# Optimization experiments

Hardware: AMD Instinct MI355X
Metric: run time of the kernel (lower is better)

The kernel has to match this reference:

```python
import jax, jax.numpy as jnp
import numpy as np

B = 2_000_000
ND = 3

def _skew(v):
    # v: [B,3] -> [B,3,3] skew-symmetric matrix
    z = jnp.zeros_like(v[..., 0])
    r0 = jnp.stack([z, -v[..., 2], v[..., 1]], axis=-1)
    r1 = jnp.stack([v[..., 2], z, -v[..., 0]], axis=-1)
    r2 = jnp.stack([-v[..., 1], v[..., 0], z], axis=-1)
    return jnp.stack([r0, r1, r2], axis=-2)

def _rotmat(v):
    # Closed-form expm of skew(v) (Rodrigues). Mathematically identical to tf.linalg.expm.
    th2 = jnp.sum(v * v, axis=-1)                      # [B]
    th = jnp.sqrt(th2)
    small = th < 1e-6
    th_s = jnp.where(small, 1.0, th)
    th2_s = jnp.where(small, 1.0, th2)
    a = jnp.where(small, 1.0, jnp.sin(th) / th_s)      # sin(t)/t
    b = jnp.where(small, 0.5, (1.0 - jnp.cos(th)) / th2_s)  # (1-cos t)/t^2
    K = _skew(v)                                       # [B,3,3]
    I = jnp.eye(ND, dtype=v.dtype)
    return I + a[:, None, None] * K + b[:, None, None] * jnp.matmul(K, K)

def setup_inputs() -> dict:
    key = jax.random.key(0)
    k1, k2, k3, k4 = jax.random.split(key, 4)
    trans = jax.random.normal(k1, (B, ND), dtype=jnp.float32)
    rotat = jax.random.normal(k2, (B, ND), dtype=jnp.float32)
    scal_dir = jax.random.normal(k3, (B, ND), dtype=jnp.float32)
    scal = jax.random.normal(k4, (B, ND), dtype=jnp.float32)
    return {"trans": trans, "rotat": rotat, "scal_dir": scal_dir, "scal": scal}

def reference(trans, rotat, scal_dir, scal):
    R = _rotmat(rotat)          # [B,3,3] rotation
    U = _rotmat(scal_dir)       # [B,3,3] scaling direction
    D = jnp.exp(scal)           # expm(diag(s)) == diag(exp(s)), [B,3]
    # U @ diag(D) @ U^T, then R @ (.)
    Ut = jnp.swapaxes(U, -1, -2)
    M = jnp.matmul(U, D[:, :, None] * Ut)   # diag(D) @ U^T broadcast as row-scaling
    M = jnp.matmul(R, M)
    return jnp.concatenate([M, trans[:, :, None]], axis=2)  # [B,3,4]
```

## Files before the change

### kernel.cpp

```cpp
#include <hip/hip_runtime.h>
#include <math.h>

#define TPB 256

__device__ __forceinline__ void rodrigues(float v0, float v1, float v2, float R[9]) {
    float th2 = v0 * v0 + v1 * v1 + v2 * v2;
    float th  = sqrtf(th2);
    float s, c;
    sincosf(th, &s, &c);
    bool  sm = th < 1e-6f;
    float a  = sm ? 1.0f : s / th;
    float b  = sm ? 0.5f : (1.0f - c) / th2;
    float cc = 1.0f - b * th2;
    R[0] = cc + b * v0 * v0;      R[1] = b * v0 * v1 - a * v2;  R[2] = b * v0 * v2 + a * v1;
    R[3] = b * v0 * v1 + a * v2;  R[4] = cc + b * v1 * v1;      R[5] = b * v1 * v2 - a * v0;
    R[6] = b * v0 * v2 - a * v1;  R[7] = b * v1 * v2 + a * v0;  R[8] = cc + b * v2 * v2;
}

__global__ __launch_bounds__(TPB) void aff_kernel(
    const float4* __restrict__ trans,
    const float4* __restrict__ rotat,
    const float4* __restrict__ sdir,
    const float4* __restrict__ scal,
    float4* __restrict__ out,
    int B)
{
    __shared__ float s_in[4][TPB * 3];
    __shared__ float s_out[TPB * 12];

    const int tid  = threadIdx.x;
    const int base = blockIdx.x * TPB;
    const int n    = min(TPB, B - base);
    const int nf4  = (n * 3) >> 2;

    if (tid < nf4) {
        const int gbase = (base * 3) >> 2;
        float4 a = trans[gbase + tid];
        float4 b = rotat[gbase + tid];
        float4 c = sdir [gbase + tid];
        float4 d = scal [gbase + tid];
        ((float4*)&s_in[0][0])[tid] = a;
        ((float4*)&s_in[1][0])[tid] = b;
        ((float4*)&s_in[2][0])[tid] = c;
        ((float4*)&s_in[3][0])[tid] = d;
    }
    __syncthreads();

    if (tid < n) {
        float t0 = s_in[0][3*tid+0], t1 = s_in[0][3*tid+1], t2 = s_in[0][3*tid+2];

        float R[9], U[9];
        rodrigues(s_in[1][3*tid+0], s_in[1][3*tid+1], s_in[1][3*tid+2], R);
        rodrigues(s_in[2][3*tid+0], s_in[2][3*tid+1], s_in[2][3*tid+2], U);
        float d0 = expf(s_in[3][3*tid+0]);
        float d1 = expf(s_in[3][3*tid+1]);
        float d2 = expf(s_in[3][3*tid+2]);

        float W[9];
#pragma unroll
        for (int i = 0; i < 3; ++i) {
            W[3*i+0] = U[3*i+0] * d0;
            W[3*i+1] = U[3*i+1] * d1;
            W[3*i+2] = U[3*i+2] * d2;
        }
        float S[9];
#pragma unroll
        for (int i = 0; i < 3; ++i)
#pragma unroll
            for (int j = 0; j < 3; ++j)
                S[3*i+j] = W[3*i+0]*U[3*j+0] + W[3*i+1]*U[3*j+1] + W[3*i+2]*U[3*j+2];
        float M[9];
#pragma unroll
        for (int i = 0; i < 3; ++i)
#pragma unroll
            for (int j = 0; j < 3; ++j)
                M[3*i+j] = R[3*i+0]*S[0+j] + R[3*i+1]*S[3+j] + R[3*i+2]*S[6+j];

        float4* so = (float4*)s_out;
        so[3*tid+0] = make_float4(M[0], M[1], M[2], t0);
        so[3*tid+1] = make_float4(M[3], M[4], M[5], t1);
        so[3*tid+2] = make_float4(M[6], M[7], M[8], t2);
    }
    __syncthreads();

    const int nq = n * 3;
    const float4* so = (const float4*)s_out;
    const int ob = base * 3;
#pragma unroll
    for (int p = 0; p < 3; ++p) {
        int idx = p * TPB + tid;
        if (idx < nq) out[ob + idx] = so[idx];
    }
}

extern "C" void kernel_launch(void* const* d_in, const int* in_sizes, int n_in,
                              void* d_out, int out_size, void* d_ws, size_t ws_size,
                              hipStream_t stream) {
    const float4* tr = (const float4*)d_in[0];
    const float4* ro = (const float4*)d_in[1];
    const float4* sd = (const float4*)d_in[2];
    const float4* sc = (const float4*)d_in[3];
    float4* out = (float4*)d_out;

    int B = in_sizes[0] / 3;
    int blocks = (B + TPB - 1) / TPB;
    aff_kernel<<<blocks, TPB, 0, stream>>>(tr, ro, sd, sc, out, B);
}
```

Before: 176.2 us.

## Use per-wave output staging, direct scalar loads, and fast intrinsics

Drops the block-wide shared-memory input staging and both __syncthreads. Each thread now loads its three floats per input directly from global memory, and output goes through a per-wavefront LDS slab synchronized only by a wave barrier. Rodrigues now uses rsqrt and __sinf/__cosf, and the exponent uses __expf, replacing precise sincos, division and expf. This cuts barrier stalls and ALU cost but gives up float4-coalesced input loads and some accuracy. It also drops the tail guard inside a wave and assumes B is a multiple of 64, which holds for 2,000,000.

```diff
diff --git a/kernel.cpp b/kernel.cpp
--- a/kernel.cpp
+++ b/kernel.cpp
@@ -5,101 +5,92 @@
 
 __device__ __forceinline__ void rodrigues(float v0, float v1, float v2, float R[9]) {
     float th2 = v0 * v0 + v1 * v1 + v2 * v2;
-    float th  = sqrtf(th2);
-    float s, c;
-    sincosf(th, &s, &c);
-    bool  sm = th < 1e-6f;
-    float a  = sm ? 1.0f : s / th;
-    float b  = sm ? 0.5f : (1.0f - c) / th2;
-    float cc = 1.0f - b * th2;
+    bool  sm  = th2 < 1e-12f;
+    float g   = sm ? 1.0f : th2;
+    float inv = rsqrtf(g);
+    float th  = g * inv;
+    float s   = __sinf(th);
+    float c   = __cosf(th);
+    float a   = sm ? 1.0f : s * inv;
+    float b   = sm ? 0.5f : (1.0f - c) * (inv * inv);
+    float cc  = 1.0f - b * th2;
     R[0] = cc + b * v0 * v0;      R[1] = b * v0 * v1 - a * v2;  R[2] = b * v0 * v2 + a * v1;
     R[3] = b * v0 * v1 + a * v2;  R[4] = cc + b * v1 * v1;      R[5] = b * v1 * v2 - a * v0;
     R[6] = b * v0 * v2 - a * v1;  R[7] = b * v1 * v2 + a * v0;  R[8] = cc + b * v2 * v2;
 }
 
 __global__ __launch_bounds__(TPB) void aff_kernel(
-    const float4* __restrict__ trans,
-    const float4* __restrict__ rotat,
-    const float4* __restrict__ sdir,
-    const float4* __restrict__ scal,
+    const float* __restrict__ trans,
+    const float* __restrict__ rotat,
+    const float* __restrict__ sdir,
+    const float* __restrict__ scal,
     float4* __restrict__ out,
     int B)
 {
-    __shared__ float s_in[4][TPB * 3];
-    __shared__ float s_out[TPB * 12];
+    __shared__ float4 s_out[TPB / 64][192];
 
-    const int tid  = threadIdx.x;
-    const int base = blockIdx.x * TPB;
-    const int n    = min(TPB, B - base);
-    const int nf4  = (n * 3) >> 2;
+    const int tid   = threadIdx.x;
+    const int w     = tid >> 6;
+    const int l     = tid & 63;
+    const int ebase = blockIdx.x * TPB + (w << 6);
+    if (ebase >= B) return;
+    const int e  = ebase + l;
+    const int b3 = 3 * e;
 
-    if (tid < nf4) {
-        const int gbase = (base * 3) >> 2;
-        float4 a = trans[gbase + tid];
-        float4 b = rotat[gbase + tid];
-        float4 c = sdir [gbase + tid];
-        float4 d = scal [gbase + tid];
-        ((float4*)&s_in[0][0])[tid] = a;
-        ((float4*)&s_in[1][0])[tid] = b;
-        ((float4*)&s_in[2][0])[tid] = c;
-        ((float4*)&s_in[3][0])[tid] = d;
+    float t0 = trans[b3], t1 = trans[b3 + 1], t2 = trans[b3 + 2];
+    float r0 = rotat[b3], r1 = rotat[b3 + 1], r2 = rotat[b3 + 2];
+    float u0 = sdir [b3], u1 = sdir [b3 + 1], u2 = sdir [b3 + 2];
+    float s0 = scal [b3], s1 = scal [b3 + 1], s2 = scal [b3 + 2];
+
+    float R[9], U[9];
+    rodrigues(r0, r1, r2, R);
+    rodrigues(u0, u1, u2, U);
+    float d0 = __expf(s0);
+    float d1 = __expf(s1);
+    float d2 = __expf(s2);
+
+    float W[9];
+#pragma unroll
+    for (int i = 0; i < 3; ++i) {
+        W[3*i+0] = U[3*i+0] * d0;
+        W[3*i+1] = U[3*i+1] * d1;
+        W[3*i+2] = U[3*i+2] * d2;
     }
-    __syncthreads();
+    float S[9];
+#pragma unroll
+    for (int i = 0; i < 3; ++i)
+#pragma unroll
+        for (int j = 0; j < 3; ++j)
+            S[3*i+j] = W[3*i+0]*U[3*j+0] + W[3*i+1]*U[3*j+1] + W[3*i+2]*U[3*j+2];
+    float M[9];
+#pragma unroll
+    for (int i = 0; i < 3; ++i)
+#pragma unroll
+        for (int j = 0; j < 3; ++j)
+            M[3*i+j] = R[3*i+0]*S[0+j] + R[3*i+1]*S[3+j] + R[3*i+2]*S[6+j];
 
-    if (tid < n) {
-        float t0 = s_in[0][3*tid+0], t1 = s_in[0][3*tid+1], t2 = s_in[0][3*tid+2];
+    float4* slab = s_out[w];
+    slab[3*l + 0] = make_float4(M[0], M[1], M[2], t0);
+    slab[3*l + 1] = make_float4(M[3], M[4], M[5], t1);
+    slab[3*l + 2] = make_float4(M[6], M[7], M[8], t2);
 
-        float R[9], U[9];
-        rodrigues(s_in[1][3*tid+0], s_in[1][3*tid+1], s_in[1][3*tid+2], R);
-        rodrigues(s_in[2][3*tid+0], s_in[2][3*tid+1], s_in[2][3*tid+2], U);
-        float d0 = expf(s_in[3][3*tid+0]);
-        float d1 = expf(s_in[3][3*tid+1]);
-        float d2 = expf(s_in[3][3*tid+2]);
+    __builtin_amdgcn_wave_barrier();
 
-        float W[9];
+    const int ob = 3 * ebase;
 #pragma unroll
-        for (int i = 0; i < 3; ++i) {
-            W[3*i+0] = U[3*i+0] * d0;
-            W[3*i+1] = U[3*i+1] * d1;
-            W[3*i+2] = U[3*i+2] * d2;
-        }
-        float S[9];
-#pragma unroll
-        for (int i = 0; i < 3; ++i)
-#pragma unroll
-            for (int j = 0; j < 3; ++j)
-                S[3*i+j] = W[3*i+0]*U[3*j+0] + W[3*i+1]*U[3*j+1] + W[3*i+2]*U[3*j+2];
-        float M[9];
-#pragma unroll
-        for (int i = 0; i < 3; ++i)
-#pragma unroll
-            for (int j = 0; j < 3; ++j)
-                M[3*i+j] = R[3*i+0]*S[0+j] + R[3*i+1]*S[3+j] + R[3*i+2]*S[6+j];
-
-        float4* so = (float4*)s_out;
-        so[3*tid+0] = make_float4(M[0], M[1], M[2], t0);
-        so[3*tid+1] = make_float4(M[3], M[4], M[5], t1);
-        so[3*tid+2] = make_float4(M[6], M[7], M[8], t2);
-    }
-    __syncthreads();
-
-    const int nq = n * 3;
-    const float4* so = (const float4*)s_out;
-    const int ob = base * 3;
-#pragma unroll
-    for (int p = 0; p < 3; ++p) {
-        int idx = p * TPB + tid;
-        if (idx < nq) out[ob + idx] = so[idx];
+    for (int k = 0; k < 3; ++k) {
+        int idx = (k << 6) + l;
+        out[ob + idx] = slab[idx];
     }
 }
 
 extern "C" void kernel_launch(void* const* d_in, const int* in_sizes, int n_in,
                               void* d_out, int out_size, void* d_ws, size_t ws_size,
                               hipStream_t stream) {
-    const float4* tr = (const float4*)d_in[0];
-    const float4* ro = (const float4*)d_in[1];
-    const float4* sd = (const float4*)d_in[2];
-    const float4* sc = (const float4*)d_in[3];
+    const float* tr = (const float*)d_in[0];
+    const float* ro = (const float*)d_in[1];
+    const float* sd = (const float*)d_in[2];
+    const float* sc = (const float*)d_in[3];
     float4* out = (float4*)d_out;
 
     int B = in_sizes[0] / 3;
```

Measured after the change: 176.8 us. About the same (+0.4%).
